# Kernel optimization log

Hardware: AMD Instinct MI355X
Metric: run time of the kernel (lower is better)

Reference implementation:

```python
import jax, jax.numpy as jnp
import numpy as np

SUPPORT = 7
NEIGHBOR = 10
EPS = 1e-12
BN_EPS = 1e-5


def knn(v, k):
    # v: (b, n, 3) -> (b, n, k) indices of k nearest (excluding self)
    sq = jnp.sum(v * v, -1)
    d = sq[:, :, None] + sq[:, None, :] - 2.0 * jnp.einsum('bnd,bmd->bnm', v, v)
    _, idx = jax.lax.top_k(-d, k + 1)
    return idx[:, :, 1:]


def gather_nb(f, idx):
    # f: (b, n, c), idx: (b, m, k) -> (b, m, k, c)
    b = f.shape[0]
    return f[jnp.arange(b)[:, None, None], idx]


def nb_dir_norm(v, idx):
    d = gather_nb(v, idx) - v[:, :, None, :]
    n = jnp.linalg.norm(d, axis=-1, keepdims=True)
    return d / jnp.maximum(n, EPS)


def norm0(d):
    n = jnp.linalg.norm(d, axis=0, keepdims=True)
    return d / jnp.maximum(n, EPS)


def conv_surface(idx, v, directions, kernel_num):
    b, n, k = idx.shape
    dn = nb_dir_norm(v, idx)
    theta = jax.nn.relu(jnp.einsum('bnkd,de->bnke', dn, norm0(directions)))
    theta = theta.reshape(b, n, k, SUPPORT, kernel_num)
    return jnp.sum(jnp.max(theta, axis=2), axis=2)  # (b, n, kernel_num)


def conv_layer(idx, v, fmap, w, bias, directions, out_ch):
    b, n, k = idx.shape
    dn = nb_dir_norm(v, idx)
    theta = jax.nn.relu(jnp.einsum('bnkd,de->bnke', dn, norm0(directions)))  # (b,n,k,s*o)
    fout = fmap @ w + bias  # (b, n, (s+1)*o)
    center = fout[..., :out_ch]
    supp = gather_nb(fout[..., out_ch:], idx)  # (b, n, k, s*o)
    act = (theta * supp).reshape(b, n, k, SUPPORT, out_ch)
    return center + jnp.sum(jnp.max(act, axis=2), axis=2)


def pool(v, f, rate, nbn, seed):
    b, n, _ = v.shape
    idx = knn(v, nbn)
    pf = jnp.max(gather_nb(f, idx), axis=2)
    m = n // rate
    samp = jax.random.permutation(jax.random.key(seed), n)[:m]
    return v[:, samp, :], pf[:, samp, :]


def nearest_idx(tgt, src):
    d = (jnp.sum(src * src, -1)[:, None, :] + jnp.sum(tgt * tgt, -1)[:, :, None]
         - 2.0 * jnp.einsum('btd,bsd->bts', tgt, src))
    return jnp.argmin(d, axis=-1)  # (b, nt)


def bn(x, g, b_, m, var):
    # per-channel over last dim (torch BN1d after transpose)
    return (x - m) / jnp.sqrt(var + BN_EPS) * g + b_


def setup_inputs() -> dict:
    key = jax.random.key(0)
    ks = jax.random.split(key, 32)
    bs, n = 4, 2048
    d = {}
    d['vertices'] = jax.random.normal(ks[0], (bs, n, 3), jnp.float32)
    d['rgb_f'] = jax.random.normal(ks[1], (bs, 32, n), jnp.float32)
    d['dir0'] = jax.random.normal(ks[2], (3, SUPPORT * 64), jnp.float32)
    def conv_params(i, cin, cout):
        s = 1.0 / np.sqrt(cin)
        w = jax.random.uniform(ks[i], (cin, (SUPPORT + 1) * cout), jnp.float32, -s, s)
        b = jax.random.uniform(ks[i + 1], ((SUPPORT + 1) * cout,), jnp.float32, -s, s)
        dr = jax.random.normal(ks[i + 2], (3, SUPPORT * cout), jnp.float32)
        return w, b, dr
    d['w1'], d['b1'], d['d1'] = conv_params(3, 128, 128)
    d['w2'], d['b2'], d['d2'] = conv_params(6, 128, 256)
    d['w3'], d['b3'], d['d3'] = conv_params(9, 256, 256)
    d['w4'], d['b4'], d['d4'] = conv_params(12, 256, 512)
    d['rgb_w'] = jax.random.normal(ks[15], (64, 32), jnp.float32) * 0.1
    d['rgb_b'] = jnp.zeros((64,), jnp.float32)
    for nm, c in [('rbn', 64), ('bn1', 128), ('bn2', 256), ('bn3', 256)]:
        d[nm + '_g'] = jnp.ones((c,), jnp.float32)
        d[nm + '_b'] = jnp.zeros((c,), jnp.float32)
        d[nm + '_m'] = jnp.zeros((c,), jnp.float32)
        d[nm + '_v'] = jnp.ones((c,), jnp.float32)
    return d


def reference(vertices, rgb_f, dir0,
              w1, b1, d1, w2, b2, d2, w3, b3, d3, w4, b4, d4,
              rgb_w, rgb_b,
              rbn_g, rbn_b, rbn_m, rbn_v,
              bn1_g, bn1_b, bn1_m, bn1_v,
              bn2_g, bn2_b, bn2_m, bn2_v,
              bn3_g, bn3_b, bn3_m, bn3_v):
    bs, n, _ = vertices.shape
    idx = knn(vertices, NEIGHBOR)
    fm0 = jax.nn.relu(conv_surface(idx, vertices, dir0, 64))  # (b, n, 64)
    # rgb_conv_1: Conv1d(32,64,1) -> ReLU -> BN
    rgb = jax.nn.relu(jnp.einsum('oc,bcn->bno', rgb_w, rgb_f) + rgb_b)  # (b, n, 64)
    rgb = bn(rgb, rbn_g, rbn_b, rbn_m, rbn_v)
    fm0 = jnp.concatenate([fm0, rgb], axis=-1)  # (b, n, 128)
    fm1 = jax.nn.relu(bn(conv_layer(idx, vertices, fm0, w1, b1, d1, 128),
                         bn1_g, bn1_b, bn1_m, bn1_v))
    v1, fp1 = pool(vertices, fm1, 4, 4, 1)  # (b, n/4, ...)
    k1 = min(NEIGHBOR, v1.shape[1] // 8)
    idx1 = knn(v1, k1)
    fm2 = jax.nn.relu(bn(conv_layer(idx1, v1, fp1, w2, b2, d2, 256),
                         bn2_g, bn2_b, bn2_m, bn2_v))
    fm3 = jax.nn.relu(bn(conv_layer(idx1, v1, fm2, w3, b3, d3, 256),
                         bn3_g, bn3_b, bn3_m, bn3_v))
    v2, fp2 = pool(v1, fm3, 4, 4, 2)  # (b, n/16, ...)
    k2 = min(NEIGHBOR, v2.shape[1] // 8)
    idx2 = knn(v2, k2)
    fm4 = conv_layer(idx2, v2, fp2, w4, b4, d4, 512)
    f_global = jnp.max(fm4, axis=1)  # (b, 512)
    ni1 = nearest_idx(vertices, v1)  # (b, n)
    ni2 = nearest_idx(vertices, v2)
    ar = jnp.arange(bs)[:, None]
    fm2u = fm2[ar, ni1]
    fm3u = fm3[ar, ni1]
    fm4u = fm4[ar, ni2]
    feat = jnp.concatenate([fm0, fm1, fm2u, fm3u, fm4u], axis=2)  # (b, n, 1280)
    fuse = jnp.concatenate([feat, jnp.broadcast_to(f_global[:, None, :], (bs, n, 512))], axis=2)
    return feat.transpose(0, 2, 1), fuse.transpose(0, 2, 1)
```

## Files before the change

kernel.cpp:

```cpp
#include <hip/hip_runtime.h>
#include <hip/hip_bf16.h>
#include <math.h>

#define NB 10
#define KNN_K 11

typedef __attribute__((ext_vector_type(8))) short bf16x8;
typedef __attribute__((ext_vector_type(4))) float f32x4;

__device__ __forceinline__ float toF(float x) { return x; }
__device__ __forceinline__ float toF(__hip_bfloat16 x) { return __bfloat162float(x); }

__device__ __forceinline__ void tf2x32(unsigned k0, unsigned k1, unsigned& x0, unsigned& x1) {
  unsigned ks0 = k0, ks1 = k1, ks2 = k0 ^ k1 ^ 0x1BD11BDAu;
  x0 += ks0; x1 += ks1;
#define TF_R(r) { x0 += x1; x1 = (x1 << (r)) | (x1 >> (32 - (r))); x1 ^= x0; }
  TF_R(13) TF_R(15) TF_R(26) TF_R(6)  x0 += ks1; x1 += ks2 + 1u;
  TF_R(17) TF_R(29) TF_R(16) TF_R(24) x0 += ks2; x1 += ks0 + 2u;
  TF_R(13) TF_R(15) TF_R(26) TF_R(6)  x0 += ks0; x1 += ks1 + 3u;
  TF_R(17) TF_R(29) TF_R(16) TF_R(24) x0 += ks1; x1 += ks2 + 4u;
  TF_R(13) TF_R(15) TF_R(26) TF_R(6)  x0 += ks2; x1 += ks0 + 5u;
#undef TF_R
}

__device__ __forceinline__ unsigned long long shfl_xor_u64(unsigned long long v, int m) {
  unsigned lo = (unsigned)v, hi = (unsigned)(v >> 32);
  lo = (unsigned)__shfl_xor((int)lo, m);
  hi = (unsigned)__shfl_xor((int)hi, m);
  return ((unsigned long long)hi << 32) | lo;
}

__global__ __launch_bounds__(1024) void perm2_kernel(int* __restrict__ samp1,
                                                     int* __restrict__ samp2) {
  __shared__ unsigned long long buf[2][2048];
  __shared__ unsigned perm[2][2048];
  int which = blockIdx.x;
  int n = (which == 0) ? 2048 : 512;
  int m = (which == 0) ? 512 : 128;
  int R = (which == 0) ? 2 : 1;
  unsigned k0 = 0u, k1 = (which == 0) ? 1u : 2u;
  int* out = (which == 0) ? samp1 : samp2;
  int T = n >> 1;
  int t = threadIdx.x;
  bool act = (t < T);
  int pb = 0;
  unsigned valA = 0, valB = 0;
  int lb = 0;
  for (int r = 0; r < R; ++r) {
    unsigned a0 = 0u, a1 = 0u, s0 = 0u, s1 = 1u;
    tf2x32(k0, k1, a0, a1);
    tf2x32(k0, k1, s0, s1);
    unsigned long long kA = 0, kB = 0;
    if (act) {
      unsigned y0 = 0u, y1 = (unsigned)t;
      tf2x32(s0, s1, y0, y1);
      kA = ((unsigned long long)(y0 ^ y1) << 32) | (unsigned)t;
      y0 = 0u; y1 = (unsigned)(t + T);
      tf2x32(s0, s1, y0, y1);
      kB = ((unsigned long long)(y0 ^ y1) << 32) | (unsigned)(t + T);
    }
    for (int kk = 2; kk <= n; kk <<= 1) {
      for (int j = kk >> 1; j > 0; j >>= 1) {
        if (j == T) {
          if (act) {
            unsigned long long lo = (kA < kB) ? kA : kB;
            unsigned long long hi = (kA < kB) ? kB : kA;
            kA = lo; kB = hi;
          }
        } else if (j >= 64) {
          if (act) { buf[lb][t] = kA; buf[lb][t + T] = kB; }
          __syncthreads();
          if (act) {
            unsigned long long okA = buf[lb][t ^ j];
            unsigned long long okB = buf[lb][(t ^ j) + T];
            bool lower = ((t & j) == 0);
            bool upA = ((t & kk) == 0);
            bool upB = (((t + T) & kk) == 0);
            kA = (upA == lower) ? (kA < okA ? kA : okA) : (kA < okA ? okA : kA);
            kB = (upB == lower) ? (kB < okB ? kB : okB) : (kB < okB ? okB : kB);
          }
          lb ^= 1;
        } else {
          unsigned long long okA = shfl_xor_u64(kA, j);
          unsigned long long okB = shfl_xor_u64(kB, j);
          if (act) {
            bool lower = ((t & j) == 0);
            bool upA = ((t & kk) == 0);
            bool upB = (((t + T) & kk) == 0);
            kA = (upA == lower) ? (kA < okA ? kA : okA) : (kA < okA ? okA : kA);
            kB = (upB == lower) ? (kB < okB ? kB : okB) : (kB < okB ? okB : kB);
          }
        }
      }
    }
    if (act) {
      unsigned posA = (unsigned)(kA & 0xffffffffu);
      unsigned posB = (unsigned)(kB & 0xffffffffu);
      if (r == 0) { valA = posA; valB = posB; }
      else        { valA = perm[pb][posA]; valB = perm[pb][posB]; }
    }
    if (r + 1 < R) {
      __syncthreads();
      if (act) { perm[pb ^ 1][t] = valA; perm[pb ^ 1][t + T] = valB; }
      pb ^= 1;
      __syncthreads();
    }
    k0 = a0; k1 = a1;
  }
  if (t < m) out[t] = (int)valA;
}

__global__ __launch_bounds__(1024) void knn_wave_kernel(const float* __restrict__ v, int N,
                                                        int* __restrict__ out) {
  __shared__ float4 pts[2048];
  int b = blockIdx.y;
  const float* vb = v + (size_t)b * N * 3;
  for (int i = threadIdx.x; i < N; i += blockDim.x) {
    float x = vb[i * 3], y = vb[i * 3 + 1], z = vb[i * 3 + 2];
    pts[i] = make_float4(x, y, z, x * x + y * y + z * z);
  }
  __syncthreads();
  int qpb = blockDim.x >> 6;
  int wave = threadIdx.x >> 6;
  int lane = threadIdx.x & 63;
  int qi = blockIdx.x * qpb + wave;
  float4 p = pts[qi];
  float bd[KNN_K]; int bi[KNN_K];
#pragma unroll
  for (int t = 0; t < KNN_K; ++t) { bd[t] = 3.4e38f; bi[t] = 0x7fffffff; }
  for (int j = lane; j < N; j += 64) {
    float4 q = pts[j];
    float dot = p.x * q.x + p.y * q.y + p.z * q.z;
    float d = p.w + q.w - 2.0f * dot;
    if (d < bd[KNN_K - 1]) {
      float cd = d; int ci = j;
#pragma unroll
      for (int t = 0; t < KNN_K; ++t) {
        bool sw = cd < bd[t];
        float td = bd[t]; int ti = bi[t];
        bd[t] = sw ? cd : td; bi[t] = sw ? ci : ti;
        cd = sw ? td : cd;   ci = sw ? ti : ci;
      }
    }
  }
  int ptr = 0;
  int* o = out + ((size_t)b * N + qi) * NB;
#pragma unroll 1
  for (int t = 0; t < KNN_K; ++t) {
    float d = (ptr < KNN_K) ? bd[ptr] : 3.4e38f;
    int idx = (ptr < KNN_K) ? bi[ptr] : 0x7fffffff;
    float rd = d; int ridx = idx;
#pragma unroll
    for (int s = 32; s > 0; s >>= 1) {
      float od = __shfl_xor(rd, s);
      int oi = __shfl_xor(ridx, s);
      if (od < rd || (od == rd && oi < ridx)) { rd = od; ridx = oi; }
    }
    if (d == rd && idx == ridx) ptr++;
    if (t >= 1 && lane == 0) o[t - 1] = ridx;
  }
}

__global__ __launch_bounds__(256) void prep_kernel(
    const float* __restrict__ w1, __hip_bfloat16* __restrict__ o1,
    const float* __restrict__ w2, __hip_bfloat16* __restrict__ o2,
    const float* __restrict__ w3, __hip_bfloat16* __restrict__ o3,
    const float* __restrict__ w4, __hip_bfloat16* __restrict__ o4,
    const float* __restrict__ s0, float* __restrict__ n0,
    const float* __restrict__ s1, float* __restrict__ n1,
    const float* __restrict__ s2, float* __restrict__ n2,
    const float* __restrict__ s3, float* __restrict__ n3,
    const float* __restrict__ s4, float* __restrict__ n4) {
  int bid = blockIdx.x;
  if (bid >= 1920) {
    int e = (bid - 1920) * 256 + threadIdx.x;
    const float* S; float* D; int W;
    if (e < 448)                          { S = s0; D = n0; W = 448; }
    else if (e < 448 + 896)               { e -= 448; S = s1; D = n1; W = 896; }
    else if (e < 448 + 896 + 1792)        { e -= 448 + 896; S = s2; D = n2; W = 1792; }
    else if (e < 448 + 896 + 3584)        { e -= 448 + 896 + 1792; S = s3; D = n3; W = 1792; }
    else if (e < 448 + 896 + 3584 + 3584) { e -= 448 + 896 + 3584; S = s4; D = n4; W = 3584; }
    else return;
    float a = S[e], b = S[W + e], c = S[2 * W + e];
    float nr = fmaxf(sqrtf(a * a + b * b + c * c), 1e-12f);
    D[e] = a / nr; D[W + e] = b / nr; D[2 * W + e] = c / nr;
    return;
  }
  __shared__ float tbuf[32][33];
  const float* W; __hip_bfloat16* O; int K, N;
  if (bid < 128)      { W = w1; O = o1; K = 128; N = 1024; }
  else if (bid < 384) { bid -= 128; W = w2; O = o2; K = 128; N = 2048; }
  else if (bid < 896) { bid -= 384; W = w3; O = o3; K = 256; N = 2048; }
  else                { bid -= 896; W = w4; O = o4; K = 256; N = 4096; }
  int tpr = N / 32;
  int tk = bid / tpr, tn = bid % tpr;
  int tx = threadIdx.x & 31, ty = threadIdx.x >> 5;
#pragma unroll
  for (int i = 0; i < 4; ++i)
    tbuf[ty + 8 * i][tx] = W[(size_t)(tk * 32 + ty + 8 * i) * N + tn * 32 + tx];
  __syncthreads();
#pragma unroll
  for (int i = 0; i < 4; ++i)
    O[(size_t)(tn * 32 + ty + 8 * i) * K + tk * 32 + tx] = __float2bfloat16(tbuf[tx][ty + 8 * i]);
}

__global__ __launch_bounds__(256) void fm0_kernel(const float* __restrict__ v, const int* __restrict__ idx,
                                                  const float* __restrict__ dir0n,
                                                  const float* __restrict__ rgb_f, const float* __restrict__ w,
                                                  const float* __restrict__ bias, const float* __restrict__ g,
                                                  const float* __restrict__ bb, const float* __restrict__ mm,
                                                  const float* __restrict__ vv,
                                                  float* __restrict__ fm0, __hip_bfloat16* __restrict__ fm0b) {
  __shared__ float dn[4][NB][3];
  int b = blockIdx.y;
  int n0 = blockIdx.x * 4;
  int tid = threadIdx.x;
  if (tid < 4 * NB) {
    int p = tid / NB, k = tid % NB;
    size_t row = (size_t)b * 2048 + (n0 + p);
    const float* c = v + row * 3;
    int nb = idx[row * NB + k];
    const float* q = v + ((size_t)b * 2048 + nb) * 3;
    float dx = q[0] - c[0], dy = q[1] - c[1], dz = q[2] - c[2];
    float nr = fmaxf(sqrtf(dx * dx + dy * dy + dz * dz), 1e-12f);
    dn[p][k][0] = dx / nr; dn[p][k][1] = dy / nr; dn[p][k][2] = dz / nr;
  }
  __syncthreads();
  int p = tid >> 6, c = tid & 63;
  int n = n0 + p;
  float acc = 0.f;
  for (int s = 0; s < 7; ++s) {
    int e = s * 64 + c;
    float d0 = dir0n[e], d1 = dir0n[448 + e], d2 = dir0n[896 + e];
    float mx = 0.f;
#pragma unroll
    for (int k = 0; k < NB; ++k) {
      float t = dn[p][k][0] * d0 + dn[p][k][1] * d1 + dn[p][k][2] * d2;
      mx = fmaxf(mx, fmaxf(t, 0.f));
    }
    acc += mx;
  }
  acc = fmaxf(acc, 0.f);
  const float* f = rgb_f + (size_t)b * 32 * 2048;
  float a2 = bias[c];
  for (int cc = 0; cc < 32; ++cc) a2 += w[c * 32 + cc] * f[cc * 2048 + n];
  a2 = fmaxf(a2, 0.f);
  a2 = (a2 - mm[c]) / sqrtf(vv[c] + 1e-5f) * g[c] + bb[c];
  size_t o = ((size_t)b * 2048 + n) * 128;
  fm0[o + c] = acc;
  fm0[o + 64 + c] = a2;
  fm0b[o + c] = __float2bfloat16(acc);
  fm0b[o + 64 + c] = __float2bfloat16(a2);
}

__global__ __launch_bounds__(256) void mfma_gemm_kernel(const __hip_bfloat16* __restrict__ A,
                                                        const __hip_bfloat16* __restrict__ BT,
                                                        const float* __restrict__ bias,
                                                        float* __restrict__ C,
                                                        __hip_bfloat16* __restrict__ Cb,
                                                        int M, int K, int N) {
  __shared__ __hip_bfloat16 Al[128 * 32];
  __shared__ __hip_bfloat16 Bl[128 * 32];
  int t = threadIdx.x;
  int l = t & 63;
  int w = t >> 6;
  int wm = w >> 1, wn = w & 1;
  int m0 = blockIdx.y * 128, n0 = blockIdx.x * 128;
  f32x4 zero = {0.f, 0.f, 0.f, 0.f};
  f32x4 acc[4][4];
#pragma unroll
  for (int i = 0; i < 4; ++i)
#pragma unroll
    for (int j = 0; j < 4; ++j) acc[i][j] = zero;

  for (int kt = 0; kt < K; kt += 32) {
#pragma unroll
    for (int j = 0; j < 2; ++j) {
      int c = t + 256 * j;
      int r = c >> 2, o = c & 3;
      *(uint4*)&Al[r * 32 + o * 8] = *(const uint4*)&A[(size_t)(m0 + r) * K + kt + o * 8];
      *(uint4*)&Bl[r * 32 + o * 8] = *(const uint4*)&BT[(size_t)(n0 + r) * K + kt + o * 8];
    }
    __syncthreads();
    bf16x8 af[4], bfv[4];
#pragma unroll
    for (int f = 0; f < 4; ++f) {
      af[f]  = *(const bf16x8*)&Al[(wm * 64 + f * 16 + (l & 15)) * 32 + (l >> 4) * 8];
      bfv[f] = *(const bf16x8*)&Bl[(wn * 64 + f * 16 + (l & 15)) * 32 + (l >> 4) * 8];
    }
#pragma unroll
    for (int i = 0; i < 4; ++i)
#pragma unroll
      for (int j = 0; j < 4; ++j)
        acc[i][j] = __builtin_amdgcn_mfma_f32_16x16x32_bf16(af[i], bfv[j], acc[i][j], 0, 0, 0);
    __syncthreads();
  }
  int col_l = l & 15, rbase = (l >> 4) * 4;
#pragma unroll
  for (int i = 0; i < 4; ++i) {
#pragma unroll
    for (int j = 0; j < 4; ++j) {
      int col = n0 + wn * 64 + j * 16 + col_l;
      float bv = bias[col];
#pragma unroll
      for (int r = 0; r < 4; ++r) {
        int m = m0 + wm * 64 + i * 16 + rbase + r;
        float val = acc[i][j][r] + bv;
        if (C)  C[(size_t)m * N + col] = val;
        if (Cb) Cb[(size_t)m * N + col] = __float2bfloat16(val);
      }
    }
  }
}

template <typename T>
__global__ __launch_bounds__(256) void conv_combine3_kernel(
    const int* __restrict__ idx, const float* __restrict__ v,
    const T* __restrict__ fout, const float* __restrict__ dirn,
    const float* __restrict__ g, const float* __restrict__ bb,
    const float* __restrict__ mm, const float* __restrict__ vv,
    int use_bn_relu, float* __restrict__ outf, __hip_bfloat16* __restrict__ outb,
    int Np, int Cout) {
  __shared__ float dnS[2][NB][3];
  __shared__ int nbS[2][NB];
  int b = blockIdx.y;
  int tid = threadIdx.x;
  int base = blockIdx.x * 256;
  int p0 = base / Cout;
  int nPts = (Cout < 256) ? 2 : 1;
  if (tid < nPts * NB) {
    int p = tid / NB, k = tid - p * NB;
    size_t prow = (size_t)b * Np + p0 + p;
    int nb = idx[prow * NB + k];
    const float* cpt = v + prow * 3;
    const float* q = v + ((size_t)b * Np + nb) * 3;
    float dx = q[0] - cpt[0], dy = q[1] - cpt[1], dz = q[2] - cpt[2];
    float nr = fmaxf(sqrtf(dx * dx + dy * dy + dz * dz), 1e-12f);
    dnS[p][k][0] = dx / nr; dnS[p][k][1] = dy / nr; dnS[p][k][2] = dz / nr;
    nbS[p][k] = b * Np + nb;
  }
  __syncthreads();
  int gid = base + tid;
  int n = gid / Cout, c = gid - n * Cout;
  int lp = n - p0;
  size_t row = (size_t)b * Np + n;
  float dn0[NB], dn1[NB], dn2[NB]; int nbr[NB];
#pragma unroll
  for (int k = 0; k < NB; ++k) {
    dn0[k] = dnS[lp][k][0]; dn1[k] = dnS[lp][k][1]; dn2[k] = dnS[lp][k][2];
    nbr[k] = nbS[lp][k];
  }
  int F = 8 * Cout, W7 = 7 * Cout;
  float acc = toF(fout[row * (size_t)F + c]);
  for (int s = 0; s < 7; ++s) {
    int e = s * Cout + c;
    float d0 = dirn[e], d1 = dirn[W7 + e], d2 = dirn[2 * W7 + e];
    float mx = -3.4e38f;
#pragma unroll
    for (int k = 0; k < NB; ++k) {
      float t = fmaxf(dn0[k] * d0 + dn1[k] * d1 + dn2[k] * d2, 0.f);
      float sv = toF(fout[(size_t)nbr[k] * F + Cout + e]);
      mx = fmaxf(mx, t * sv);
    }
    acc += mx;
  }
  if (use_bn_relu) {
    acc = (acc - mm[c]) / sqrtf(vv[c] + 1e-5f) * g[c] + bb[c];
    acc = fmaxf(acc, 0.f);
  }
  outf[row * (size_t)Cout + c] = acc;
  if (outb) outb[row * (size_t)Cout + c] = __float2bfloat16(acc);
}

__global__ void pool_kernel(const float* __restrict__ v, const float* __restrict__ fm,
                            const int* __restrict__ idx10, const int* __restrict__ samp,
                            float* __restrict__ v_out, float* __restrict__ f_out,
                            __hip_bfloat16* __restrict__ f_out_b, int Nin, int C) {
  int b = blockIdx.y, mi = blockIdx.x, c = threadIdx.x;
  int n = samp[mi];
  size_t row = (size_t)b * Nin + n;
  float mx = -3.4e38f;
#pragma unroll
  for (int j = 0; j < 4; ++j) {
    int nb = idx10[row * NB + j];
    mx = fmaxf(mx, fm[((size_t)b * Nin + nb) * C + c]);
  }
  int Mout = gridDim.x;
  f_out[((size_t)b * Mout + mi) * C + c] = mx;
  f_out_b[((size_t)b * Mout + mi) * C + c] = __float2bfloat16(mx);
  if (c < 3) v_out[((size_t)b * Mout + mi) * 3 + c] = v[row * 3 + c];
}

__global__ __launch_bounds__(256) void nearest3_kernel(const float* __restrict__ tgt,
                                                       const float* __restrict__ v1,
                                                       const float* __restrict__ v2,
                                                       const float* __restrict__ fm4,
                                                       int* __restrict__ ni1, int* __restrict__ ni2,
                                                       float* __restrict__ fg) {
  __shared__ float4 sp[512];
  int z = blockIdx.z;
  int b = blockIdx.y;
  if (z == 2) {
    if (blockIdx.x >= 2) return;
    int c = blockIdx.x * 256 + threadIdx.x;
    float mx = -3.4e38f;
    for (int p = 0; p < 128; ++p) mx = fmaxf(mx, fm4[((size_t)b * 128 + p) * 512 + c]);
    fg[b * 512 + c] = mx;
    return;
  }
  const float* src = z ? v2 : v1;
  int S = z ? 128 : 512;
  int* out = z ? ni2 : ni1;
  for (int i = threadIdx.x; i < S; i += blockDim.x) {
    const float* q = src + ((size_t)b * S + i) * 3;
    float x = q[0], y = q[1], zz = q[2];
    sp[i] = make_float4(x, y, zz, x * x + y * y + zz * zz);
  }
  __syncthreads();
  int wave = threadIdx.x >> 6, lane = threadIdx.x & 63;
  int n = blockIdx.x * 4 + wave;
  const float* t = tgt + ((size_t)b * 2048 + n) * 3;
  float x = t[0], y = t[1], zz = t[2];
  float sqt = x * x + y * y + zz * zz;
  float best = 3.4e38f; int bi = 0x7fffffff;
  for (int s = lane; s < S; s += 64) {
    float4 q = sp[s];
    float d = q.w + sqt - 2.f * (x * q.x + y * q.y + zz * q.z);
    if (d < best) { best = d; bi = s; }
  }
#pragma unroll
  for (int m = 32; m > 0; m >>= 1) {
    float od = __shfl_xor(best, m);
    int oi = __shfl_xor(bi, m);
    if (od < best || (od == best && oi < bi)) { best = od; bi = oi; }
  }
  if (lane == 0) out[(size_t)b * 2048 + n] = bi;
}

__global__ __launch_bounds__(256) void output2_kernel(
    const float* __restrict__ fm0, const float* __restrict__ fm1,
    const float* __restrict__ fm2, const float* __restrict__ fm3,
    const float* __restrict__ fm4, const float* __restrict__ fg,
    const int* __restrict__ ni1, const int* __restrict__ ni2,
    float* __restrict__ out) {
  __shared__ float tile[64][33];
  __shared__ int srow[64];
  int b = blockIdx.z;
  int cc0 = blockIdx.y * 32;
  int n0 = blockIdx.x * 64;
  int tid = threadIdx.x;
  const float* P; int Cs, coff, mode;
  if (cc0 < 128)       { P = fm0; Cs = 128; coff = cc0;        mode = 0; }
  else if (cc0 < 256)  { P = fm1; Cs = 128; coff = cc0 - 128;  mode = 0; }
  else if (cc0 < 512)  { P = fm2; Cs = 256; coff = cc0 - 256;  mode = 1; }
  else if (cc0 < 768)  { P = fm3; Cs = 256; coff = cc0 - 512;  mode = 1; }
  else if (cc0 < 1280) { P = fm4; Cs = 512; coff = cc0 - 768;  mode = 2; }
  else                 { P = fg;  Cs = 512; coff = cc0 - 1280; mode = 3; }
  if (tid < 64) {
    int n = n0 + tid;
    size_t r2 = (size_t)b * 2048 + n;
    int sr;
    if (mode == 0)      sr = b * 2048 + n;
    else if (mode == 1) sr = b * 512 + ni1[r2];
    else if (mode == 2) sr = b * 128 + ni2[r2];
    else                sr = b;
    srow[tid] = sr;
  }
  __syncthreads();
  int tx = tid & 31, ty = tid >> 5;
#pragma unroll
  for (int r = 0; r < 8; ++r) {
    int nl = ty + 8 * r;
    tile[nl][tx] = P[(size_t)srow[nl] * Cs + coff + tx];
  }
  __syncthreads();
  int lx = tid & 63, ly = tid >> 6;
  float* out0 = out;
  float* out1 = out + (size_t)4 * 1280 * 2048;
#pragma unroll
  for (int ci = 0; ci < 8; ++ci) {
    int cl = ly + 4 * ci;
    int cc = cc0 + cl;
    float vv = tile[lx][cl];
    out1[((size_t)b * 1792 + cc) * 2048 + n0 + lx] = vv;
    if (cc < 1280) out0[((size_t)b * 1280 + cc) * 2048 + n0 + lx] = vv;
  }
}

extern "C" void kernel_launch(void* const* d_in, const int* in_sizes, int n_in,
                              void* d_out, int out_size, void* d_ws, size_t ws_size,
                              hipStream_t stream) {
  (void)in_sizes; (void)n_in; (void)out_size; (void)ws_size;
  const float* vertices = (const float*)d_in[0];
  const float* rgb_f    = (const float*)d_in[1];
  const float* dir0     = (const float*)d_in[2];
  const float* w1 = (const float*)d_in[3],  *b1 = (const float*)d_in[4],  *d1 = (const float*)d_in[5];
  const float* w2 = (const float*)d_in[6],  *b2 = (const float*)d_in[7],  *d2 = (const float*)d_in[8];
  const float* w3 = (const float*)d_in[9],  *b3 = (const float*)d_in[10], *d3 = (const float*)d_in[11];
  const float* w4 = (const float*)d_in[12], *b4 = (const float*)d_in[13], *d4 = (const float*)d_in[14];
  const float* rgb_w = (const float*)d_in[15], *rgb_b = (const float*)d_in[16];
  const float* rbn_g = (const float*)d_in[17], *rbn_b = (const float*)d_in[18];
  const float* rbn_m = (const float*)d_in[19], *rbn_v = (const float*)d_in[20];
  const float* bn1_g = (const float*)d_in[21], *bn1_b = (const float*)d_in[22];
  const float* bn1_m = (const float*)d_in[23], *bn1_v = (const float*)d_in[24];
  const float* bn2_g = (const float*)d_in[25], *bn2_b = (const float*)d_in[26];
  const float* bn2_m = (const float*)d_in[27], *bn2_v = (const float*)d_in[28];
  const float* bn3_g = (const float*)d_in[29], *bn3_b = (const float*)d_in[30];
  const float* bn3_m = (const float*)d_in[31], *bn3_v = (const float*)d_in[32];
  float* out = (float*)d_out;

  char* ws = (char*)d_ws;
  size_t off = 0;
  auto alloc = [&](size_t bytes) -> void* {
    void* p = ws + off;
    off += (bytes + 255) & ~(size_t)255;
    return p;
  };
  int*   samp1 = (int*)alloc(512 * 4);
  int*   samp2 = (int*)alloc(128 * 4);
  int*   idx0  = (int*)alloc((size_t)4 * 2048 * NB * 4);
  int*   idx1  = (int*)alloc((size_t)4 * 512 * NB * 4);
  int*   idx2  = (int*)alloc((size_t)4 * 128 * NB * 4);
  float* fm0   = (float*)alloc((size_t)4 * 2048 * 128 * 4);
  float* fm1   = (float*)alloc((size_t)4 * 2048 * 128 * 4);
  float* fout  = (float*)alloc((size_t)4 * 2048 * 1024 * 4);
  __hip_bfloat16* foutb = (__hip_bfloat16*)alloc((size_t)4 * 2048 * 1024 * 2);
  float* v1    = (float*)alloc((size_t)4 * 512 * 3 * 4);
  float* fp1   = (float*)alloc((size_t)4 * 512 * 128 * 4);
  float* fm2   = (float*)alloc((size_t)4 * 512 * 256 * 4);
  float* fm3   = (float*)alloc((size_t)4 * 512 * 256 * 4);
  float* v2    = (float*)alloc((size_t)4 * 128 * 3 * 4);
  float* fp2   = (float*)alloc((size_t)4 * 128 * 256 * 4);
  float* fm4   = (float*)alloc((size_t)4 * 128 * 512 * 4);
  float* fg    = (float*)alloc((size_t)4 * 512 * 4);
  int*   ni1   = (int*)alloc((size_t)4 * 2048 * 4);
  int*   ni2   = (int*)alloc((size_t)4 * 2048 * 4);
  __hip_bfloat16* fm0b = (__hip_bfloat16*)alloc((size_t)4 * 2048 * 128 * 2);
  __hip_bfloat16* fp1b = (__hip_bfloat16*)alloc((size_t)4 * 512 * 128 * 2);
  __hip_bfloat16* fm2b = (__hip_bfloat16*)alloc((size_t)4 * 512 * 256 * 2);
  __hip_bfloat16* fp2b = (__hip_bfloat16*)alloc((size_t)4 * 128 * 256 * 2);
  __hip_bfloat16* wt1  = (__hip_bfloat16*)alloc((size_t)1024 * 128 * 2);
  __hip_bfloat16* wt2  = (__hip_bfloat16*)alloc((size_t)2048 * 128 * 2);
  __hip_bfloat16* wt3  = (__hip_bfloat16*)alloc((size_t)2048 * 256 * 2);
  __hip_bfloat16* wt4  = (__hip_bfloat16*)alloc((size_t)4096 * 256 * 2);
  float* d0n = (float*)alloc((size_t)3 * 448 * 4);
  float* d1n = (float*)alloc((size_t)3 * 896 * 4);
  float* d2n = (float*)alloc((size_t)3 * 1792 * 4);
  float* d3n = (float*)alloc((size_t)3 * 1792 * 4);
  float* d4n = (float*)alloc((size_t)3 * 3584 * 4);

  prep_kernel<<<1954, 256, 0, stream>>>(w1, wt1, w2, wt2, w3, wt3, w4, wt4,
                                        dir0, d0n, d1, d1n, d2, d2n, d3, d3n, d4, d4n);
  perm2_kernel<<<2, 1024, 0, stream>>>(samp1, samp2);

  knn_wave_kernel<<<dim3(2048 / 16, 4), 1024, 0, stream>>>(vertices, 2048, idx0);

  fm0_kernel<<<dim3(512, 4), 256, 0, stream>>>(vertices, idx0, d0n, rgb_f, rgb_w, rgb_b,
                                               rbn_g, rbn_b, rbn_m, rbn_v, fm0, fm0b);

  mfma_gemm_kernel<<<dim3(1024 / 128, 8192 / 128), 256, 0, stream>>>(fm0b, wt1, b1, nullptr, foutb, 8192, 128, 1024);
  conv_combine3_kernel<__hip_bfloat16><<<dim3(2048 * 128 / 256, 4), 256, 0, stream>>>(idx0, vertices, foutb, d1n,
      bn1_g, bn1_b, bn1_m, bn1_v, 1, fm1, nullptr, 2048, 128);

  pool_kernel<<<dim3(512, 4), 128, 0, stream>>>(vertices, fm1, idx0, samp1, v1, fp1, fp1b, 2048, 128);
  knn_wave_kernel<<<dim3(512 / 4, 4), 256, 0, stream>>>(v1, 512, idx1);

  mfma_gemm_kernel<<<dim3(2048 / 128, 2048 / 128), 256, 0, stream>>>(fp1b, wt2, b2, nullptr, foutb, 2048, 128, 2048);
  conv_combine3_kernel<__hip_bfloat16><<<dim3(512 * 256 / 256, 4), 256, 0, stream>>>(idx1, v1, foutb, d2n,
      bn2_g, bn2_b, bn2_m, bn2_v, 1, fm2, fm2b, 512, 256);
  mfma_gemm_kernel<<<dim3(2048 / 128, 2048 / 128), 256, 0, stream>>>(fm2b, wt3, b3, nullptr, foutb, 2048, 256, 2048);
  conv_combine3_kernel<__hip_bfloat16><<<dim3(512 * 256 / 256, 4), 256, 0, stream>>>(idx1, v1, foutb, d3n,
      bn3_g, bn3_b, bn3_m, bn3_v, 1, fm3, nullptr, 512, 256);

  pool_kernel<<<dim3(128, 4), 256, 0, stream>>>(v1, fm3, idx1, samp2, v2, fp2, fp2b, 512, 256);
  knn_wave_kernel<<<dim3(128 / 4, 4), 256, 0, stream>>>(v2, 128, idx2);

  mfma_gemm_kernel<<<dim3(4096 / 128, 512 / 128), 256, 0, stream>>>(fp2b, wt4, b4, fout, nullptr, 512, 256, 4096);
  conv_combine3_kernel<float><<<dim3(128 * 512 / 256, 4), 256, 0, stream>>>(idx2, v2, fout, d4n,
      nullptr, nullptr, nullptr, nullptr, 0, fm4, nullptr, 128, 512);

  nearest3_kernel<<<dim3(512, 4, 3), 256, 0, stream>>>(vertices, v1, v2, fm4, ni1, ni2, fg);

  output2_kernel<<<dim3(32, 56, 4), 256, 0, stream>>>(fm0, fm1, fm2, fm3, fm4, fg, ni1, ni2, out);
}
```

Before: 297.1 us.

## Merge setup kernels, hoist nearest-index search early, fuse global max into output

```diff
diff --git a/kernel.cpp b/kernel.cpp
--- a/kernel.cpp
+++ b/kernel.cpp
@@ -30,138 +30,7 @@
   return ((unsigned long long)hi << 32) | lo;
 }
 
-__global__ __launch_bounds__(1024) void perm2_kernel(int* __restrict__ samp1,
-                                                     int* __restrict__ samp2) {
-  __shared__ unsigned long long buf[2][2048];
-  __shared__ unsigned perm[2][2048];
-  int which = blockIdx.x;
-  int n = (which == 0) ? 2048 : 512;
-  int m = (which == 0) ? 512 : 128;
-  int R = (which == 0) ? 2 : 1;
-  unsigned k0 = 0u, k1 = (which == 0) ? 1u : 2u;
-  int* out = (which == 0) ? samp1 : samp2;
-  int T = n >> 1;
-  int t = threadIdx.x;
-  bool act = (t < T);
-  int pb = 0;
-  unsigned valA = 0, valB = 0;
-  int lb = 0;
-  for (int r = 0; r < R; ++r) {
-    unsigned a0 = 0u, a1 = 0u, s0 = 0u, s1 = 1u;
-    tf2x32(k0, k1, a0, a1);
-    tf2x32(k0, k1, s0, s1);
-    unsigned long long kA = 0, kB = 0;
-    if (act) {
-      unsigned y0 = 0u, y1 = (unsigned)t;
-      tf2x32(s0, s1, y0, y1);
-      kA = ((unsigned long long)(y0 ^ y1) << 32) | (unsigned)t;
-      y0 = 0u; y1 = (unsigned)(t + T);
-      tf2x32(s0, s1, y0, y1);
-      kB = ((unsigned long long)(y0 ^ y1) << 32) | (unsigned)(t + T);
-    }
-    for (int kk = 2; kk <= n; kk <<= 1) {
-      for (int j = kk >> 1; j > 0; j >>= 1) {
-        if (j == T) {
-          if (act) {
-            unsigned long long lo = (kA < kB) ? kA : kB;
-            unsigned long long hi = (kA < kB) ? kB : kA;
-            kA = lo; kB = hi;
-          }
-        } else if (j >= 64) {
-          if (act) { buf[lb][t] = kA; buf[lb][t + T] = kB; }
-          __syncthreads();
-          if (act) {
-            unsigned long long okA = buf[lb][t ^ j];
-            unsigned long long okB = buf[lb][(t ^ j) + T];
-            bool lower = ((t & j) == 0);
-            bool upA = ((t & kk) == 0);
-            bool upB = (((t + T) & kk) == 0);
-            kA = (upA == lower) ? (kA < okA ? kA : okA) : (kA < okA ? okA : kA);
-            kB = (upB == lower) ? (kB < okB ? kB : okB) : (kB < okB ? okB : kB);
-          }
-          lb ^= 1;
-        } else {
-          unsigned long long okA = shfl_xor_u64(kA, j);
-          unsigned long long okB = shfl_xor_u64(kB, j);
-          if (act) {
-            bool lower = ((t & j) == 0);
-            bool upA = ((t & kk) == 0);
-            bool upB = (((t + T) & kk) == 0);
-            kA = (upA == lower) ? (kA < okA ? kA : okA) : (kA < okA ? okA : kA);
-            kB = (upB == lower) ? (kB < okB ? kB : okB) : (kB < okB ? okB : kB);
-          }
-        }
-      }
-    }
-    if (act) {
-      unsigned posA = (unsigned)(kA & 0xffffffffu);
-      unsigned posB = (unsigned)(kB & 0xffffffffu);
-      if (r == 0) { valA = posA; valB = posB; }
-      else        { valA = perm[pb][posA]; valB = perm[pb][posB]; }
-    }
-    if (r + 1 < R) {
-      __syncthreads();
-      if (act) { perm[pb ^ 1][t] = valA; perm[pb ^ 1][t + T] = valB; }
-      pb ^= 1;
-      __syncthreads();
-    }
-    k0 = a0; k1 = a1;
-  }
-  if (t < m) out[t] = (int)valA;
-}
-
-__global__ __launch_bounds__(1024) void knn_wave_kernel(const float* __restrict__ v, int N,
-                                                        int* __restrict__ out) {
-  __shared__ float4 pts[2048];
-  int b = blockIdx.y;
-  const float* vb = v + (size_t)b * N * 3;
-  for (int i = threadIdx.x; i < N; i += blockDim.x) {
-    float x = vb[i * 3], y = vb[i * 3 + 1], z = vb[i * 3 + 2];
-    pts[i] = make_float4(x, y, z, x * x + y * y + z * z);
-  }
-  __syncthreads();
-  int qpb = blockDim.x >> 6;
-  int wave = threadIdx.x >> 6;
-  int lane = threadIdx.x & 63;
-  int qi = blockIdx.x * qpb + wave;
-  float4 p = pts[qi];
-  float bd[KNN_K]; int bi[KNN_K];
-#pragma unroll
-  for (int t = 0; t < KNN_K; ++t) { bd[t] = 3.4e38f; bi[t] = 0x7fffffff; }
-  for (int j = lane; j < N; j += 64) {
-    float4 q = pts[j];
-    float dot = p.x * q.x + p.y * q.y + p.z * q.z;
-    float d = p.w + q.w - 2.0f * dot;
-    if (d < bd[KNN_K - 1]) {
-      float cd = d; int ci = j;
-#pragma unroll
-      for (int t = 0; t < KNN_K; ++t) {
-        bool sw = cd < bd[t];
-        float td = bd[t]; int ti = bi[t];
-        bd[t] = sw ? cd : td; bi[t] = sw ? ci : ti;
-        cd = sw ? td : cd;   ci = sw ? ti : ci;
-      }
-    }
-  }
-  int ptr = 0;
-  int* o = out + ((size_t)b * N + qi) * NB;
-#pragma unroll 1
-  for (int t = 0; t < KNN_K; ++t) {
-    float d = (ptr < KNN_K) ? bd[ptr] : 3.4e38f;
-    int idx = (ptr < KNN_K) ? bi[ptr] : 0x7fffffff;
-    float rd = d; int ridx = idx;
-#pragma unroll
-    for (int s = 32; s > 0; s >>= 1) {
-      float od = __shfl_xor(rd, s);
-      int oi = __shfl_xor(ridx, s);
-      if (od < rd || (od == rd && oi < ridx)) { rd = od; ridx = oi; }
-    }
-    if (d == rd && idx == ridx) ptr++;
-    if (t >= 1 && lane == 0) o[t - 1] = ridx;
-  }
-}
-
-__global__ __launch_bounds__(256) void prep_kernel(
+__global__ __launch_bounds__(1024) void setup_kernel(
     const float* __restrict__ w1, __hip_bfloat16* __restrict__ o1,
     const float* __restrict__ w2, __hip_bfloat16* __restrict__ o2,
     const float* __restrict__ w3, __hip_bfloat16* __restrict__ o3,
@@ -170,10 +39,34 @@
     const float* __restrict__ s1, float* __restrict__ n1,
     const float* __restrict__ s2, float* __restrict__ n2,
     const float* __restrict__ s3, float* __restrict__ n3,
-    const float* __restrict__ s4, float* __restrict__ n4) {
+    const float* __restrict__ s4, float* __restrict__ n4,
+    int* __restrict__ samp1, int* __restrict__ samp2,
+    const float* __restrict__ v, int* __restrict__ idx0) {
+  __shared__ __align__(16) char smem[49152];
   int bid = blockIdx.x;
-  if (bid >= 1920) {
-    int e = (bid - 1920) * 256 + threadIdx.x;
+  if (bid < 480) {
+    int sub = threadIdx.x >> 8, t = threadIdx.x & 255;
+    int wtile = bid * 4 + sub;
+    float (*tbuf)[33] = (float(*)[33])(smem + sub * (32 * 33 * 4));
+    const float* W; __hip_bfloat16* O; int K, N;
+    if (wtile < 128)      { W = w1; O = o1; K = 128; N = 1024; }
+    else if (wtile < 384) { wtile -= 128; W = w2; O = o2; K = 128; N = 2048; }
+    else if (wtile < 896) { wtile -= 384; W = w3; O = o3; K = 256; N = 2048; }
+    else                  { wtile -= 896; W = w4; O = o4; K = 256; N = 4096; }
+    int tpr = N / 32;
+    int tk = wtile / tpr, tn = wtile % tpr;
+    int tx = t & 31, ty = t >> 5;
+#pragma unroll
+    for (int i = 0; i < 4; ++i)
+      tbuf[ty + 8 * i][tx] = W[(size_t)(tk * 32 + ty + 8 * i) * N + tn * 32 + tx];
+    __syncthreads();
+#pragma unroll
+    for (int i = 0; i < 4; ++i)
+      O[(size_t)(tn * 32 + ty + 8 * i) * K + tk * 32 + tx] = __float2bfloat16(tbuf[tx][ty + 8 * i]);
+    return;
+  }
+  if (bid < 489) {
+    int e = (bid - 480) * 1024 + threadIdx.x;
     const float* S; float* D; int W;
     if (e < 448)                          { S = s0; D = n0; W = 448; }
     else if (e < 448 + 896)               { e -= 448; S = s1; D = n1; W = 896; }
@@ -186,35 +79,233 @@
     D[e] = a / nr; D[W + e] = b / nr; D[2 * W + e] = c / nr;
     return;
   }
-  __shared__ float tbuf[32][33];
-  const float* W; __hip_bfloat16* O; int K, N;
-  if (bid < 128)      { W = w1; O = o1; K = 128; N = 1024; }
-  else if (bid < 384) { bid -= 128; W = w2; O = o2; K = 128; N = 2048; }
-  else if (bid < 896) { bid -= 384; W = w3; O = o3; K = 256; N = 2048; }
-  else                { bid -= 896; W = w4; O = o4; K = 256; N = 4096; }
-  int tpr = N / 32;
-  int tk = bid / tpr, tn = bid % tpr;
-  int tx = threadIdx.x & 31, ty = threadIdx.x >> 5;
-#pragma unroll
-  for (int i = 0; i < 4; ++i)
-    tbuf[ty + 8 * i][tx] = W[(size_t)(tk * 32 + ty + 8 * i) * N + tn * 32 + tx];
+  if (bid < 491) {
+    unsigned long long (*buf)[2048] = (unsigned long long(*)[2048])smem;
+    unsigned (*perm)[2048] = (unsigned(*)[2048])(smem + 32768);
+    int which = bid - 489;
+    int n = (which == 0) ? 2048 : 512;
+    int m = (which == 0) ? 512 : 128;
+    int R = (which == 0) ? 2 : 1;
+    unsigned k0 = 0u, k1 = (which == 0) ? 1u : 2u;
+    int* out = (which == 0) ? samp1 : samp2;
+    int T = n >> 1;
+    int t = threadIdx.x;
+    bool act = (t < T);
+    int pb = 0;
+    unsigned valA = 0, valB = 0;
+    int lb = 0;
+    for (int r = 0; r < R; ++r) {
+      unsigned a0 = 0u, a1 = 0u, ss0 = 0u, ss1 = 1u;
+      tf2x32(k0, k1, a0, a1);
+      tf2x32(k0, k1, ss0, ss1);
+      unsigned long long kA = 0, kB = 0;
+      if (act) {
+        unsigned y0 = 0u, y1 = (unsigned)t;
+        tf2x32(ss0, ss1, y0, y1);
+        kA = ((unsigned long long)(y0 ^ y1) << 32) | (unsigned)t;
+        y0 = 0u; y1 = (unsigned)(t + T);
+        tf2x32(ss0, ss1, y0, y1);
+        kB = ((unsigned long long)(y0 ^ y1) << 32) | (unsigned)(t + T);
+      }
+      for (int kk = 2; kk <= n; kk <<= 1) {
+        for (int j = kk >> 1; j > 0; j >>= 1) {
+          if (j == T) {
+            if (act) {
+              unsigned long long lo = (kA < kB) ? kA : kB;
+              unsigned long long hi = (kA < kB) ? kB : kA;
+              kA = lo; kB = hi;
+            }
+          } else if (j >= 64) {
+            if (act) { buf[lb][t] = kA; buf[lb][t + T] = kB; }
+            __syncthreads();
+            if (act) {
+              unsigned long long okA = buf[lb][t ^ j];
+              unsigned long long okB = buf[lb][(t ^ j) + T];
+              bool lower = ((t & j) == 0);
+              bool upA = ((t & kk) == 0);
+              bool upB = (((t + T) & kk) == 0);
+              kA = (upA == lower) ? (kA < okA ? kA : okA) : (kA < okA ? okA : kA);
+              kB = (upB == lower) ? (kB < okB ? kB : okB) : (kB < okB ? okB : kB);
+            }
+            lb ^= 1;
+          } else {
+            unsigned long long okA = shfl_xor_u64(kA, j);
+            unsigned long long okB = shfl_xor_u64(kB, j);
+            if (act) {
+              bool lower = ((t & j) == 0);
+              bool upA = ((t & kk) == 0);
+              bool upB = (((t + T) & kk) == 0);
+              kA = (upA == lower) ? (kA < okA ? kA : okA) : (kA < okA ? okA : kA);
+              kB = (upB == lower) ? (kB < okB ? kB : okB) : (kB < okB ? okB : kB);
+            }
+          }
+        }
+      }
+      if (act) {
+        unsigned posA = (unsigned)(kA & 0xffffffffu);
+        unsigned posB = (unsigned)(kB & 0xffffffffu);
+        if (r == 0) { valA = posA; valB = posB; }
+        else        { valA = perm[pb][posA]; valB = perm[pb][posB]; }
+      }
+      if (r + 1 < R) {
+        __syncthreads();
+        if (act) { perm[pb ^ 1][t] = valA; perm[pb ^ 1][t + T] = valB; }
+        pb ^= 1;
+        __syncthreads();
+      }
+      k0 = a0; k1 = a1;
+    }
+    if (t < m) out[t] = (int)valA;
+    return;
+  }
+  {
+    float4* pts = (float4*)smem;
+    int i = bid - 491;
+    int b = i >> 7, x = i & 127;
+    const int N = 2048;
+    const float* vb = v + (size_t)b * N * 3;
+    for (int i2 = threadIdx.x; i2 < N; i2 += 1024) {
+      float xx = vb[i2 * 3], yy = vb[i2 * 3 + 1], zz = vb[i2 * 3 + 2];
+      pts[i2] = make_float4(xx, yy, zz, xx * xx + yy * yy + zz * zz);
+    }
+    __syncthreads();
+    int wave = threadIdx.x >> 6;
+    int lane = threadIdx.x & 63;
+    int qi = x * 16 + wave;
+    float4 p = pts[qi];
+    float bd[KNN_K]; int bi[KNN_K];
+#pragma unroll
+    for (int t = 0; t < KNN_K; ++t) { bd[t] = 3.4e38f; bi[t] = 0x7fffffff; }
+    for (int j = lane; j < N; j += 64) {
+      float4 q = pts[j];
+      float dot = p.x * q.x + p.y * q.y + p.z * q.z;
+      float d = p.w + q.w - 2.0f * dot;
+      if (d < bd[KNN_K - 1]) {
+        float cd = d; int ci = j;
+#pragma unroll
+        for (int t = 0; t < KNN_K; ++t) {
+          bool sw = cd < bd[t];
+          float td = bd[t]; int ti = bi[t];
+          bd[t] = sw ? cd : td; bi[t] = sw ? ci : ti;
+          cd = sw ? td : cd;   ci = sw ? ti : ci;
+        }
+      }
+    }
+    int ptr = 0;
+    int* o = idx0 + ((size_t)b * N + qi) * NB;
+#pragma unroll 1
+    for (int t = 0; t < KNN_K; ++t) {
+      float d = (ptr < KNN_K) ? bd[ptr] : 3.4e38f;
+      int idx = (ptr < KNN_K) ? bi[ptr] : 0x7fffffff;
+      float rd = d; int ridx = idx;
+#pragma unroll
+      for (int s = 32; s > 0; s >>= 1) {
+        float od = __shfl_xor(rd, s);
+        int oi = __shfl_xor(ridx, s);
+        if (od < rd || (od == rd && oi < ridx)) { rd = od; ridx = oi; }
+      }
+      if (d == rd && idx == ridx) ptr++;
+      if (t >= 1 && lane == 0) o[t - 1] = ridx;
+    }
+  }
+}
+
+__global__ __launch_bounds__(1024) void knn_wave_kernel(const float* __restrict__ v, int N,
+                                                        int* __restrict__ out) {
+  __shared__ float4 pts[2048];
+  int b = blockIdx.y;
+  const float* vb = v + (size_t)b * N * 3;
+  for (int i = threadIdx.x; i < N; i += blockDim.x) {
+    float x = vb[i * 3], y = vb[i * 3 + 1], z = vb[i * 3 + 2];
+    pts[i] = make_float4(x, y, z, x * x + y * y + z * z);
+  }
   __syncthreads();
-#pragma unroll
-  for (int i = 0; i < 4; ++i)
-    O[(size_t)(tn * 32 + ty + 8 * i) * K + tk * 32 + tx] = __float2bfloat16(tbuf[tx][ty + 8 * i]);
-}
-
-__global__ __launch_bounds__(256) void fm0_kernel(const float* __restrict__ v, const int* __restrict__ idx,
-                                                  const float* __restrict__ dir0n,
-                                                  const float* __restrict__ rgb_f, const float* __restrict__ w,
-                                                  const float* __restrict__ bias, const float* __restrict__ g,
-                                                  const float* __restrict__ bb, const float* __restrict__ mm,
-                                                  const float* __restrict__ vv,
-                                                  float* __restrict__ fm0, __hip_bfloat16* __restrict__ fm0b) {
+  int qpb = blockDim.x >> 6;
+  int wave = threadIdx.x >> 6;
+  int lane = threadIdx.x & 63;
+  int qi = blockIdx.x * qpb + wave;
+  float4 p = pts[qi];
+  float bd[KNN_K]; int bi[KNN_K];
+#pragma unroll
+  for (int t = 0; t < KNN_K; ++t) { bd[t] = 3.4e38f; bi[t] = 0x7fffffff; }
+  for (int j = lane; j < N; j += 64) {
+    float4 q = pts[j];
+    float dot = p.x * q.x + p.y * q.y + p.z * q.z;
+    float d = p.w + q.w - 2.0f * dot;
+    if (d < bd[KNN_K - 1]) {
+      float cd = d; int ci = j;
+#pragma unroll
+      for (int t = 0; t < KNN_K; ++t) {
+        bool sw = cd < bd[t];
+        float td = bd[t]; int ti = bi[t];
+        bd[t] = sw ? cd : td; bi[t] = sw ? ci : ti;
+        cd = sw ? td : cd;   ci = sw ? ti : ci;
+      }
+    }
+  }
+  int ptr = 0;
+  int* o = out + ((size_t)b * N + qi) * NB;
+#pragma unroll 1
+  for (int t = 0; t < KNN_K; ++t) {
+    float d = (ptr < KNN_K) ? bd[ptr] : 3.4e38f;
+    int idx = (ptr < KNN_K) ? bi[ptr] : 0x7fffffff;
+    float rd = d; int ridx = idx;
+#pragma unroll
+    for (int s = 32; s > 0; s >>= 1) {
+      float od = __shfl_xor(rd, s);
+      int oi = __shfl_xor(ridx, s);
+      if (od < rd || (od == rd && oi < ridx)) { rd = od; ridx = oi; }
+    }
+    if (d == rd && idx == ridx) ptr++;
+    if (t >= 1 && lane == 0) o[t - 1] = ridx;
+  }
+}
+
+__global__ __launch_bounds__(256) void fm0n_kernel(const float* __restrict__ v, const int* __restrict__ idx,
+                                                   const float* __restrict__ dir0n,
+                                                   const float* __restrict__ rgb_f, const float* __restrict__ w,
+                                                   const float* __restrict__ bias, const float* __restrict__ g,
+                                                   const float* __restrict__ bb, const float* __restrict__ mm,
+                                                   const float* __restrict__ vv,
+                                                   const int* __restrict__ samp1, const int* __restrict__ samp2,
+                                                   float* __restrict__ fm0, __hip_bfloat16* __restrict__ fm0b,
+                                                   int* __restrict__ ni1, int* __restrict__ ni2) {
+  int z = blockIdx.z;
+  int b = blockIdx.y;
+  int tid = threadIdx.x;
+  if (z >= 1) {
+    __shared__ float4 sp[512];
+    int S = (z == 1) ? 512 : 128;
+    int* outp = (z == 1) ? ni1 : ni2;
+    for (int i = tid; i < S; i += blockDim.x) {
+      int src = (z == 1) ? samp1[i] : samp1[samp2[i]];
+      const float* q = v + ((size_t)b * 2048 + src) * 3;
+      float x = q[0], y = q[1], zz = q[2];
+      sp[i] = make_float4(x, y, zz, x * x + y * y + zz * zz);
+    }
+    __syncthreads();
+    int wave = tid >> 6, lane = tid & 63;
+    int n = blockIdx.x * 4 + wave;
+    const float* t = v + ((size_t)b * 2048 + n) * 3;
+    float x = t[0], y = t[1], zz = t[2];
+    float sqt = x * x + y * y + zz * zz;
+    float best = 3.4e38f; int bi = 0x7fffffff;
+    for (int s = lane; s < S; s += 64) {
+      float4 q = sp[s];
+      float d = q.w + sqt - 2.f * (x * q.x + y * q.y + zz * q.z);
+      if (d < best) { best = d; bi = s; }
+    }
+#pragma unroll
+    for (int m = 32; m > 0; m >>= 1) {
+      float od = __shfl_xor(best, m);
+      int oi = __shfl_xor(bi, m);
+      if (od < best || (od == best && oi < bi)) { best = od; bi = oi; }
+    }
+    if (lane == 0) outp[(size_t)b * 2048 + n] = bi;
+    return;
+  }
   __shared__ float dn[4][NB][3];
-  int b = blockIdx.y;
   int n0 = blockIdx.x * 4;
-  int tid = threadIdx.x;
   if (tid < 4 * NB) {
     int p = tid / NB, k = tid % NB;
     size_t row = (size_t)b * 2048 + (n0 + p);
@@ -391,56 +482,10 @@
   if (c < 3) v_out[((size_t)b * Mout + mi) * 3 + c] = v[row * 3 + c];
 }
 
-__global__ __launch_bounds__(256) void nearest3_kernel(const float* __restrict__ tgt,
-                                                       const float* __restrict__ v1,
-                                                       const float* __restrict__ v2,
-                                                       const float* __restrict__ fm4,
-                                                       int* __restrict__ ni1, int* __restrict__ ni2,
-                                                       float* __restrict__ fg) {
-  __shared__ float4 sp[512];
-  int z = blockIdx.z;
-  int b = blockIdx.y;
-  if (z == 2) {
-    if (blockIdx.x >= 2) return;
-    int c = blockIdx.x * 256 + threadIdx.x;
-    float mx = -3.4e38f;
-    for (int p = 0; p < 128; ++p) mx = fmaxf(mx, fm4[((size_t)b * 128 + p) * 512 + c]);
-    fg[b * 512 + c] = mx;
-    return;
-  }
-  const float* src = z ? v2 : v1;
-  int S = z ? 128 : 512;
-  int* out = z ? ni2 : ni1;
-  for (int i = threadIdx.x; i < S; i += blockDim.x) {
-    const float* q = src + ((size_t)b * S + i) * 3;
-    float x = q[0], y = q[1], zz = q[2];
-    sp[i] = make_float4(x, y, zz, x * x + y * y + zz * zz);
-  }
-  __syncthreads();
-  int wave = threadIdx.x >> 6, lane = threadIdx.x & 63;
-  int n = blockIdx.x * 4 + wave;
-  const float* t = tgt + ((size_t)b * 2048 + n) * 3;
-  float x = t[0], y = t[1], zz = t[2];
-  float sqt = x * x + y * y + zz * zz;
-  float best = 3.4e38f; int bi = 0x7fffffff;
-  for (int s = lane; s < S; s += 64) {
-    float4 q = sp[s];
-    float d = q.w + sqt - 2.f * (x * q.x + y * q.y + zz * q.z);
-    if (d < best) { best = d; bi = s; }
-  }
-#pragma unroll
-  for (int m = 32; m > 0; m >>= 1) {
-    float od = __shfl_xor(best, m);
-    int oi = __shfl_xor(bi, m);
-    if (od < best || (od == best && oi < bi)) { best = od; bi = oi; }
-  }
-  if (lane == 0) out[(size_t)b * 2048 + n] = bi;
-}
-
-__global__ __launch_bounds__(256) void output2_kernel(
+__global__ __launch_bounds__(256) void output3_kernel(
     const float* __restrict__ fm0, const float* __restrict__ fm1,
     const float* __restrict__ fm2, const float* __restrict__ fm3,
-    const float* __restrict__ fm4, const float* __restrict__ fg,
+    const float* __restrict__ fm4,
     const int* __restrict__ ni1, const int* __restrict__ ni2,
     float* __restrict__ out) {
   __shared__ float tile[64][33];
@@ -449,21 +494,46 @@
   int cc0 = blockIdx.y * 32;
   int n0 = blockIdx.x * 64;
   int tid = threadIdx.x;
+  float* out0 = out;
+  float* out1 = out + (size_t)4 * 1280 * 2048;
+  if (cc0 >= 1280) {
+    __shared__ float red[8][32];
+    __shared__ float fgv[32];
+    int coff = cc0 - 1280;
+    int tx = tid & 31, ty = tid >> 5;
+    float pm = -3.4e38f;
+    for (int p = ty; p < 128; p += 8)
+      pm = fmaxf(pm, fm4[((size_t)b * 128 + p) * 512 + coff + tx]);
+    red[ty][tx] = pm;
+    __syncthreads();
+    if (tid < 32) {
+      float m = red[0][tid];
+#pragma unroll
+      for (int r = 1; r < 8; ++r) m = fmaxf(m, red[r][tid]);
+      fgv[tid] = m;
+    }
+    __syncthreads();
+    int lx = tid & 63, ly = tid >> 6;
+#pragma unroll
+    for (int ci = 0; ci < 8; ++ci) {
+      int cl = ly + 4 * ci;
+      out1[((size_t)b * 1792 + cc0 + cl) * 2048 + n0 + lx] = fgv[cl];
+    }
+    return;
+  }
   const float* P; int Cs, coff, mode;
   if (cc0 < 128)       { P = fm0; Cs = 128; coff = cc0;        mode = 0; }
   else if (cc0 < 256)  { P = fm1; Cs = 128; coff = cc0 - 128;  mode = 0; }
   else if (cc0 < 512)  { P = fm2; Cs = 256; coff = cc0 - 256;  mode = 1; }
   else if (cc0 < 768)  { P = fm3; Cs = 256; coff = cc0 - 512;  mode = 1; }
-  else if (cc0 < 1280) { P = fm4; Cs = 512; coff = cc0 - 768;  mode = 2; }
-  else                 { P = fg;  Cs = 512; coff = cc0 - 1280; mode = 3; }
+  else                 { P = fm4; Cs = 512; coff = cc0 - 768;  mode = 2; }
   if (tid < 64) {
     int n = n0 + tid;
     size_t r2 = (size_t)b * 2048 + n;
     int sr;
     if (mode == 0)      sr = b * 2048 + n;
     else if (mode == 1) sr = b * 512 + ni1[r2];
-    else if (mode == 2) sr = b * 128 + ni2[r2];
-    else                sr = b;
+    else                sr = b * 128 + ni2[r2];
     srow[tid] = sr;
   }
   __syncthreads();
@@ -475,15 +545,13 @@
   }
   __syncthreads();
   int lx = tid & 63, ly = tid >> 6;
-  float* out0 = out;
-  float* out1 = out + (size_t)4 * 1280 * 2048;
 #pragma unroll
   for (int ci = 0; ci < 8; ++ci) {
     int cl = ly + 4 * ci;
     int cc = cc0 + cl;
     float vv = tile[lx][cl];
     out1[((size_t)b * 1792 + cc) * 2048 + n0 + lx] = vv;
-    if (cc < 1280) out0[((size_t)b * 1280 + cc) * 2048 + n0 + lx] = vv;
+    out0[((size_t)b * 1280 + cc) * 2048 + n0 + lx] = vv;
   }
 }
 
@@ -532,7 +600,6 @@
   float* v2    = (float*)alloc((size_t)4 * 128 * 3 * 4);
   float* fp2   = (float*)alloc((size_t)4 * 128 * 256 * 4);
   float* fm4   = (float*)alloc((size_t)4 * 128 * 512 * 4);
-  float* fg    = (float*)alloc((size_t)4 * 512 * 4);
   int*   ni1   = (int*)alloc((size_t)4 * 2048 * 4);
   int*   ni2   = (int*)alloc((size_t)4 * 2048 * 4);
   __hip_bfloat16* fm0b = (__hip_bfloat16*)alloc((size_t)4 * 2048 * 128 * 2);
@@ -549,14 +616,13 @@
   float* d3n = (float*)alloc((size_t)3 * 1792 * 4);
   float* d4n = (float*)alloc((size_t)3 * 3584 * 4);
 
-  prep_kernel<<<1954, 256, 0, stream>>>(w1, wt1, w2, wt2, w3, wt3, w4, wt4,
-                                        dir0, d0n, d1, d1n, d2, d2n, d3, d3n, d4, d4n);
-  perm2_kernel<<<2, 1024, 0, stream>>>(samp1, samp2);
-
-  knn_wave_kernel<<<dim3(2048 / 16, 4), 1024, 0, stream>>>(vertices, 2048, idx0);
-
-  fm0_kernel<<<dim3(512, 4), 256, 0, stream>>>(vertices, idx0, d0n, rgb_f, rgb_w, rgb_b,
-                                               rbn_g, rbn_b, rbn_m, rbn_v, fm0, fm0b);
+  setup_kernel<<<1003, 1024, 0, stream>>>(w1, wt1, w2, wt2, w3, wt3, w4, wt4,
+                                          dir0, d0n, d1, d1n, d2, d2n, d3, d3n, d4, d4n,
+                                          samp1, samp2, vertices, idx0);
+
+  fm0n_kernel<<<dim3(512, 4, 3), 256, 0, stream>>>(vertices, idx0, d0n, rgb_f, rgb_w, rgb_b,
+                                                   rbn_g, rbn_b, rbn_m, rbn_v, samp1, samp2,
+                                                   fm0, fm0b, ni1, ni2);
 
   mfma_gemm_kernel<<<dim3(1024 / 128, 8192 / 128), 256, 0, stream>>>(fm0b, wt1, b1, nullptr, foutb, 8192, 128, 1024);
   conv_combine3_kernel<__hip_bfloat16><<<dim3(2048 * 128 / 256, 4), 256, 0, stream>>>(idx0, vertices, foutb, d1n,
@@ -579,7 +645,5 @@
   conv_combine3_kernel<float><<<dim3(128 * 512 / 256, 4), 256, 0, stream>>>(idx2, v2, fout, d4n,
       nullptr, nullptr, nullptr, nullptr, 0, fm4, nullptr, 128, 512);
 
-  nearest3_kernel<<<dim3(512, 4, 3), 256, 0, stream>>>(vertices, v1, v2, fm4, ni1, ni2, fg);
-
-  output2_kernel<<<dim3(32, 56, 4), 256, 0, stream>>>(fm0, fm1, fm2, fm3, fm4, fg, ni1, ni2, out);
-}
+  output3_kernel<<<dim3(32, 56, 4), 256, 0, stream>>>(fm0, fm1, fm2, fm3, fm4, ni1, ni2, out);
+}
```

New measurement: 245.3 us (median of 2 runs). -17.4%, faster.
